# Kernel optimization log

Hardware: AMD Instinct MI355X
Metric: run time of the kernel (lower is better)

The kernel has to match this reference:

```python
import jax, jax.numpy as jnp
import numpy as np

HEAD = 16
EMD = 1024
QK = 64
V = 64
B, SQ, SKV = 4, 2048, 2048


def setup_inputs() -> dict:
    key = jax.random.key(0)
    ks = jax.random.split(key, 10)
    s = 0.02
    return {
        "x_q": jax.random.normal(ks[0], (B, SQ, EMD), dtype=jnp.float32),
        "x_k_v": jax.random.normal(ks[1], (B, SKV, EMD), dtype=jnp.float32),
        "mask_pad": jax.random.randint(ks[2], (B, SQ, SKV), 0, 2) > 0,
        # torch nn.Linear weights: [out_features, in_features]
        "Wq_w": jax.random.normal(ks[3], (QK * HEAD, EMD), dtype=jnp.float32) * s,
        "Wq_b": jnp.zeros((QK * HEAD,), dtype=jnp.float32),
        "Wk_w": jax.random.normal(ks[4], (QK * HEAD, EMD), dtype=jnp.float32) * s,
        "Wk_b": jnp.zeros((QK * HEAD,), dtype=jnp.float32),
        "Wv_w": jax.random.normal(ks[5], (V * HEAD, EMD), dtype=jnp.float32) * s,
        "Wv_b": jnp.zeros((V * HEAD,), dtype=jnp.float32),
    }


def reference(x_q, x_k_v, mask_pad, Wq_w, Wq_b, Wk_w, Wk_b, Wv_w, Wv_b):
    b, sq, _ = x_q.shape
    skv = x_k_v.shape[1]
    q = x_q @ Wq_w.T + Wq_b            # [B, SQ, H*QK]
    k = x_k_v @ Wk_w.T + Wk_b          # [B, SKV, H*QK]
    v = x_k_v @ Wv_w.T + Wv_b          # [B, SKV, H*V]
    q = q.reshape(b, sq, HEAD, QK).transpose(0, 2, 1, 3)   # [B, H, SQ, QK]
    k = k.reshape(b, skv, HEAD, QK).transpose(0, 2, 1, 3)  # [B, H, SKV, QK]
    v = v.reshape(b, skv, HEAD, V).transpose(0, 2, 1, 3)   # [B, H, SKV, V]
    scale = 1.0 / jnp.sqrt(jnp.float32(QK))
    atten = jnp.einsum('bhqd,bhkd->bhqk', q, k) * scale    # [B, H, SQ, SKV]
    atten = jnp.where(mask_pad[:, None, :, :], jnp.float32(-1e9), atten)
    atten = jax.nn.softmax(atten, axis=-1)
    z = jnp.einsum('bhqk,bhkv->bhqv', atten, v)            # [B, H, SQ, V]
    z = z.transpose(0, 2, 1, 3).reshape(b, sq, HEAD * V)   # [B, SQ, H*V]
    return z
```

## Files before the change

kernel.cpp:

```cpp
#include <hip/hip_runtime.h>
#include <stdint.h>

#define HEADS 16
#define EMDIM 1024
#define DHEAD 64
#define BATCH 4
#define SEQQ 2048
#define SEQK 2048
#define NT (SEQK / 64)
#define QSCALE 0.18033688011112042f

typedef __attribute__((ext_vector_type(8))) short bf16x8;
typedef __attribute__((ext_vector_type(4))) float f32x4;
typedef __attribute__((ext_vector_type(4))) unsigned int u32x4;

typedef __attribute__((address_space(3))) void lds_void;
typedef const __attribute__((address_space(1))) void gbl_void;
#define GL_LDS16(g, l) __builtin_amdgcn_global_load_lds((gbl_void*)(g), (lds_void*)(l), 16, 0, 0)
#define MFMA16(a, b, c) __builtin_amdgcn_mfma_f32_16x16x32_bf16(a, b, c, 0, 0, 0)

__device__ __forceinline__ unsigned short f2bf(float f) {
    unsigned int u = __builtin_bit_cast(unsigned int, f);
    u += 0x7fffu + ((u >> 16) & 1u);
    return (unsigned short)(u >> 16);
}

__device__ __forceinline__ void exp2x4(float& a, float& b, float& c, float& d) {
    asm("v_exp_f32 %0, %0\n\t"
        "v_exp_f32 %1, %1\n\t"
        "v_exp_f32 %2, %2\n\t"
        "v_exp_f32 %3, %3\n\t"
        "s_nop 0"
        : "+v"(a), "+v"(b), "+v"(c), "+v"(d));
}

__device__ __forceinline__ unsigned int cvtpk_bf16(float lo, float hi) {
    unsigned int r;
    asm("v_cvt_pk_bf16_f32 %0, %1, %2" : "=v"(r) : "v"(lo), "v"(hi));
    return r;
}

__global__ __launch_bounds__(256) void prep_all(const float* __restrict__ xq,
                                                const float* __restrict__ xkv,
                                                const float* __restrict__ wq,
                                                const float* __restrict__ wk,
                                                const float* __restrict__ wv,
                                                unsigned short* __restrict__ oxq,
                                                unsigned short* __restrict__ oxkv,
                                                unsigned short* __restrict__ owq,
                                                unsigned short* __restrict__ owk,
                                                unsigned short* __restrict__ owv,
                                                const void* __restrict__ mask,
                                                unsigned long long* __restrict__ packed) {
    const int NX = (BATCH * SEQQ * EMDIM) / 4;
    const int NW = (EMDIM * EMDIM) / 4;
    const int total = 2 * NX + 3 * NW;
    for (int i = blockIdx.x * 256 + threadIdx.x; i < total; i += gridDim.x * 256) {
        const float* src;
        unsigned short* dst;
        int j = i;
        if (j < NX) { src = xq; dst = oxq; }
        else if ((j -= NX) < NX) { src = xkv; dst = oxkv; }
        else if ((j -= NX) < NW) { src = wq; dst = owq; }
        else if ((j -= NW) < NW) { src = wk; dst = owk; }
        else { j -= NW; src = wv; dst = owv; }
        float4 v = reinterpret_cast<const float4*>(src)[j];
        ushort4 o;
        o.x = f2bf(v.x); o.y = f2bf(v.y); o.z = f2bf(v.z); o.w = f2bf(v.w);
        reinterpret_cast<ushort4*>(dst)[j] = o;
    }
    const int* mi = (const int*)mask;
    const uint8_t* mu = (const uint8_t*)mask;
    const int lane = threadIdx.x & 63;
    const bool u8src = __any(((unsigned)mi[lane]) > 1u);
    const size_t N = (size_t)BATCH * SEQQ * SEQK;
    const size_t stride = (size_t)gridDim.x * blockDim.x;
    for (size_t idx = (size_t)blockIdx.x * blockDim.x + threadIdx.x; idx < N; idx += stride) {
        const int v = u8src ? (int)mu[idx] : mi[idx];
        const unsigned long long bb = __ballot(v != 0);
        if (lane == 0) packed[idx >> 6] = bb;
    }
}

__global__ __launch_bounds__(256) void gemm_qkv(
    const unsigned short* __restrict__ xq, const unsigned short* __restrict__ xkv,
    const unsigned short* __restrict__ Wqm, const unsigned short* __restrict__ Wkm,
    const unsigned short* __restrict__ Wvm,
    const float* __restrict__ bq, const float* __restrict__ bk, const float* __restrict__ bv,
    unsigned short* __restrict__ Qo, unsigned short* __restrict__ Ko,
    unsigned short* __restrict__ Vo) {
    __shared__ __align__(16) unsigned short Alds[128 * 64];
    __shared__ __align__(16) unsigned short Blds[128 * 64];
    const int nb = blockIdx.x;
    const int which = nb >> 3;
    const unsigned short* A = (which == 0) ? xq : xkv;
    const unsigned short* W = (which == 0) ? Wqm : (which == 1) ? Wkm : Wvm;
    const float* bias = (which == 0) ? bq : (which == 1) ? bk : bv;
    const int n0 = (nb & 7) * 128;
    const int m0 = blockIdx.y * 128;

    const int tid = threadIdx.x;
    const int lane = tid & 63;
    const int wid = tid >> 6;
    const int wm = wid >> 1, wn = wid & 1;
    const int lq = lane & 15, lh = lane >> 4;

    f32x4 acc[4][4] = {};

    const int srow = tid >> 3;
    const int scol = (tid & 7) * 8;

    for (int kt = 0; kt < 16; ++kt) {
        const int kb = kt * 64;
#pragma unroll
        for (int i = 0; i < 4; ++i) {
            const int row = i * 32 + srow;
            GL_LDS16(&A[(size_t)(m0 + row) * EMDIM + kb + scol], &Alds[row * 64 + scol]);
            GL_LDS16(&W[(size_t)(n0 + row) * EMDIM + kb + scol], &Blds[row * 64 + scol]);
        }
        __syncthreads();
#pragma unroll
        for (int ks = 0; ks < 2; ++ks) {
            bf16x8 af[4], bfr[4];
#pragma unroll
            for (int mf = 0; mf < 4; ++mf)
                af[mf] = *(const bf16x8*)&Alds[(wm * 64 + mf * 16 + lq) * 64 + ks * 32 + lh * 8];
#pragma unroll
            for (int nf = 0; nf < 4; ++nf)
                bfr[nf] = *(const bf16x8*)&Blds[(wn * 64 + nf * 16 + lq) * 64 + ks * 32 + lh * 8];
#pragma unroll
            for (int mf = 0; mf < 4; ++mf)
#pragma unroll
                for (int nf = 0; nf < 4; ++nf)
                    acc[mf][nf] = MFMA16(af[mf], bfr[nf], acc[mf][nf]);
        }
        __syncthreads();
    }

#pragma unroll
    for (int nf = 0; nf < 4; ++nf) {
        const int n = n0 + wn * 64 + nf * 16 + lq;
        const float bvv = bias[n];
        const int h = n >> 6, d = n & 63;
#pragma unroll
        for (int mf = 0; mf < 4; ++mf) {
            const int mbase = m0 + wm * 64 + mf * 16 + lh * 4;
            const int b = mbase >> 11;
            const int s = mbase & 2047;
            if (which == 2) {
                ushort4 pk;
                pk.x = f2bf(acc[mf][nf][0] + bvv);
                pk.y = f2bf(acc[mf][nf][1] + bvv);
                pk.z = f2bf(acc[mf][nf][2] + bvv);
                pk.w = f2bf(acc[mf][nf][3] + bvv);
                *(ushort4*)&Vo[(((size_t)(b * HEADS + h) * DHEAD) + d) * SEQK + s] = pk;
            } else {
                const float sc = (which == 0) ? QSCALE : 1.0f;
                unsigned short* o = (which == 0) ? Qo : Ko;
#pragma unroll
                for (int r = 0; r < 4; ++r) {
                    float v = (acc[mf][nf][r] + bvv) * sc;
                    o[(((size_t)(b * HEADS + h) * SEQQ) + (s + r)) * DHEAD + d] = f2bf(v);
                }
            }
        }
    }
}

__global__ __launch_bounds__(256, 3) void attn_fused(const unsigned short* __restrict__ Q,
                                                     const unsigned short* __restrict__ K,
                                                     const unsigned short* __restrict__ VT,
                                                     const unsigned long long* __restrict__ mpk,
                                                     float* __restrict__ out) {
    const int tid = threadIdx.x;
    const int lane = tid & 63;
    const int wid = tid >> 6;
    const int lq = lane & 15, lh = lane >> 4;
    const int bh = blockIdx.x;
    const int b = bh >> 4, h = bh & 15;
    const int qbase = blockIdx.y * 128 + wid * 32;

    __shared__ __align__(16) unsigned short Kl[2][64 * 64];
    __shared__ __align__(16) unsigned short Vl[2][64 * 64];

    const unsigned short* Kbh = K + (size_t)bh * SEQK * DHEAD;
    const unsigned short* Vbh = VT + (size_t)bh * DHEAD * SEQK;

    bf16x8 bq[2][2];
    const unsigned long long* mrow[2];
#pragma unroll
    for (int sub = 0; sub < 2; ++sub) {
        const int q = qbase + sub * 16 + lq;
        const unsigned short* qrow = Q + ((size_t)bh * SEQQ + q) * DHEAD;
        bq[sub][0] = *(const bf16x8*)&qrow[lh * 8];
        bq[sub][1] = *(const bf16x8*)&qrow[32 + lh * 8];
        mrow[sub] = mpk + ((size_t)b * SEQQ + q) * NT;
    }

    f32x4 acc[4][2] = {};
    f32x4 accl[2] = {};

    const bf16x8 vone = {16256, 16256, 16256, 16256, 16256, 16256, 16256, 16256};

    const int srow8 = lane >> 3;
    const int sg = (lane & 7) ^ srow8;
    const int g7 = lq & 7;

    auto stage = [&](int s, int t) {
        const int k0 = t * 64;
#pragma unroll
        for (int i = 0; i < 2; ++i) {
            const int cc = wid * 2 + i;
            const int r = cc * 8 + srow8;
            GL_LDS16(Kbh + (size_t)(k0 + r) * DHEAD + sg * 8, &Kl[s][cc * 512]);
            GL_LDS16(Vbh + (size_t)r * SEQK + k0 + sg * 8, &Vl[s][cc * 512]);
        }
    };

    unsigned long long mwc[2], mwn[2];
#pragma unroll
    for (int sub = 0; sub < 2; ++sub) mwc[sub] = mrow[sub][0];

    stage(0, 0);
    __syncthreads();
    int cur = 0;

    for (int t = 0; t < NT; ++t) {
        if (t < NT - 1) {
            stage(cur ^ 1, t + 1);
#pragma unroll
            for (int sub = 0; sub < 2; ++sub) mwn[sub] = mrow[sub][t + 1];
        }

        uint2 w[2][4];
#pragma unroll
        for (int kb = 0; kb < 4; ++kb) {
            const unsigned short* kr = &Kl[cur][(kb * 16 + lq) * 64];
            const bf16x8 a0 = *(const bf16x8*)&kr[((0 + lh) ^ g7) * 8];
            const bf16x8 a1 = *(const bf16x8*)&kr[((4 + lh) ^ g7) * 8];
#pragma unroll
            for (int sub = 0; sub < 2; ++sub) {
                f32x4 z = {};
                z = MFMA16(a0, bq[sub][0], z);
                z = MFMA16(a1, bq[sub][1], z);
                const unsigned int ml = (unsigned int)(mwc[sub] >> (kb * 16 + lh * 4));
                float p0 = (ml & 1u) ? -1e9f : z[0];
                float p1 = (ml & 2u) ? -1e9f : z[1];
                float p2 = (ml & 4u) ? -1e9f : z[2];
                float p3 = (ml & 8u) ? -1e9f : z[3];
                exp2x4(p0, p1, p2, p3);
                w[sub][kb].x = cvtpk_bf16(p0, p1);
                w[sub][kb].y = cvtpk_bf16(p2, p3);
            }
        }

        bf16x8 pf[2][2];
#pragma unroll
        for (int sub = 0; sub < 2; ++sub) {
#pragma unroll
            for (int ks = 0; ks < 2; ++ks) {
                unsigned int s0 = w[sub][2 * ks].x, s2 = w[sub][2 * ks + 1].x;
                unsigned int s1 = w[sub][2 * ks].y, s3 = w[sub][2 * ks + 1].y;
                asm("v_permlane32_swap_b32 %0, %1" : "+v"(s0), "+v"(s2));
                asm("v_permlane32_swap_b32 %0, %1" : "+v"(s1), "+v"(s3));
                asm("v_permlane16_swap_b32 %0, %1" : "+v"(s0), "+v"(s2));
                asm("v_permlane16_swap_b32 %0, %1" : "+v"(s1), "+v"(s3));
                u32x4 fd = {s0, s1, s2, s3};
                pf[sub][ks] = __builtin_bit_cast(bf16x8, fd);
            }
        }

        __builtin_amdgcn_s_setprio(1);
#pragma unroll
        for (int sub = 0; sub < 2; ++sub) {
            accl[sub] = MFMA16(vone, pf[sub][0], accl[sub]);
            accl[sub] = MFMA16(vone, pf[sub][1], accl[sub]);
        }
#pragma unroll
        for (int vb = 0; vb < 4; ++vb) {
            const unsigned short* vr = &Vl[cur][(vb * 16 + lq) * 64];
            const bf16x8 av0 = *(const bf16x8*)&vr[((0 + lh) ^ g7) * 8];
            const bf16x8 av1 = *(const bf16x8*)&vr[((4 + lh) ^ g7) * 8];
#pragma unroll
            for (int sub = 0; sub < 2; ++sub) {
                acc[vb][sub] = MFMA16(av0, pf[sub][0], acc[vb][sub]);
                acc[vb][sub] = MFMA16(av1, pf[sub][1], acc[vb][sub]);
            }
        }
        __builtin_amdgcn_s_setprio(0);

        __syncthreads();
        cur ^= 1;
#pragma unroll
        for (int sub = 0; sub < 2; ++sub) mwc[sub] = mwn[sub];
    }

#pragma unroll
    for (int sub = 0; sub < 2; ++sub) {
        const float rl = 1.f / accl[sub][0];
        const int q = qbase + sub * 16 + lq;
        float* orow = out + ((size_t)b * SEQQ + q) * (HEADS * DHEAD) + h * DHEAD;
#pragma unroll
        for (int vb = 0; vb < 4; ++vb) {
            float4 o4;
            o4.x = acc[vb][sub][0] * rl;
            o4.y = acc[vb][sub][1] * rl;
            o4.z = acc[vb][sub][2] * rl;
            o4.w = acc[vb][sub][3] * rl;
            *(float4*)&orow[vb * 16 + lh * 4] = o4;
        }
    }
}

extern "C" void kernel_launch(void* const* d_in, const int* in_sizes, int n_in,
                              void* d_out, int out_size, void* d_ws, size_t ws_size,
                              hipStream_t stream) {
    const float* x_q  = (const float*)d_in[0];
    const float* x_kv = (const float*)d_in[1];
    const void*  mask = (const void*)d_in[2];
    const float* Wq_w = (const float*)d_in[3];
    const float* Wq_b = (const float*)d_in[4];
    const float* Wk_w = (const float*)d_in[5];
    const float* Wk_b = (const float*)d_in[6];
    const float* Wv_w = (const float*)d_in[7];
    const float* Wv_b = (const float*)d_in[8];
    float* out = (float*)d_out;

    char* ws = (char*)d_ws;
    const size_t SZ_QKV = (size_t)BATCH * HEADS * SEQQ * DHEAD * sizeof(unsigned short);
    const size_t SZ_X   = (size_t)BATCH * SEQQ * EMDIM * sizeof(unsigned short);
    const size_t SZ_W   = (size_t)EMDIM * EMDIM * sizeof(unsigned short);
    unsigned short* Qb  = (unsigned short*)(ws);
    unsigned short* Kb  = (unsigned short*)(ws + SZ_QKV);
    unsigned short* VTb = (unsigned short*)(ws + 2 * SZ_QKV);
    unsigned short* xqb = (unsigned short*)(ws + 3 * SZ_QKV);
    unsigned short* xkb = (unsigned short*)(ws + 3 * SZ_QKV + SZ_X);
    unsigned short* Wqb = (unsigned short*)(ws + 3 * SZ_QKV + 2 * SZ_X);
    unsigned short* Wkb = (unsigned short*)(ws + 3 * SZ_QKV + 2 * SZ_X + SZ_W);
    unsigned short* Wvb = (unsigned short*)(ws + 3 * SZ_QKV + 2 * SZ_X + 2 * SZ_W);
    unsigned long long* mpk = (unsigned long long*)(ws + 3 * SZ_QKV + 2 * SZ_X + 3 * SZ_W);

    prep_all<<<2048, 256, 0, stream>>>(x_q, x_kv, Wq_w, Wk_w, Wv_w, xqb, xkb, Wqb, Wkb, Wvb,
                                       mask, mpk);

    dim3 ggrid(24, BATCH * SEQQ / 128);
    gemm_qkv<<<ggrid, 256, 0, stream>>>(xqb, xkb, Wqb, Wkb, Wvb, Wq_b, Wk_b, Wv_b, Qb, Kb, VTb);

    dim3 agrid(BATCH * HEADS, SEQQ / 128);
    attn_fused<<<agrid, 256, 0, stream>>>(Qb, Kb, VTb, mpk, out);
}
```

Before: 219.3 us.

## Stage Q/K GEMM epilogue through swizzled LDS and remap blocks across XCDs

The Q and K outputs of the QKV projection GEMM are now written into a swizzled LDS tile first and then stored to global memory as 16-byte vectors per row. Previously each lane wrote scattered 2-byte values. Block IDs are also remapped so that consecutive M tiles land on different XCDs while N tiles of the same M tile share an XCD, aiming for better L2 reuse of the A rows. This adds an extra barrier and LDS round trip in the epilogue. The remap assumes a grid of 24 by the number of M tiles and a multiple of 8 XCDs.

```diff
diff --git a/kernel.cpp b/kernel.cpp
--- a/kernel.cpp
+++ b/kernel.cpp
@@ -89,15 +89,19 @@
     const float* __restrict__ bq, const float* __restrict__ bk, const float* __restrict__ bv,
     unsigned short* __restrict__ Qo, unsigned short* __restrict__ Ko,
     unsigned short* __restrict__ Vo) {
-    __shared__ __align__(16) unsigned short Alds[128 * 64];
-    __shared__ __align__(16) unsigned short Blds[128 * 64];
-    const int nb = blockIdx.x;
+    __shared__ __align__(16) unsigned short Tlds[2][128 * 64];
+
+    const int rawid = blockIdx.y * gridDim.x + blockIdx.x;
+    const int xcd = rawid & 7;
+    const int slot = rawid >> 3;
+    const int nb = slot % 24;
+    const int mt = (slot / 24) * 8 + xcd;
+    const int m0 = mt * 128;
     const int which = nb >> 3;
     const unsigned short* A = (which == 0) ? xq : xkv;
     const unsigned short* W = (which == 0) ? Wqm : (which == 1) ? Wkm : Wvm;
     const float* bias = (which == 0) ? bq : (which == 1) ? bk : bv;
     const int n0 = (nb & 7) * 128;
-    const int m0 = blockIdx.y * 128;
 
     const int tid = threadIdx.x;
     const int lane = tid & 63;
@@ -115,8 +119,8 @@
 #pragma unroll
         for (int i = 0; i < 4; ++i) {
             const int row = i * 32 + srow;
-            GL_LDS16(&A[(size_t)(m0 + row) * EMDIM + kb + scol], &Alds[row * 64 + scol]);
-            GL_LDS16(&W[(size_t)(n0 + row) * EMDIM + kb + scol], &Blds[row * 64 + scol]);
+            GL_LDS16(&A[(size_t)(m0 + row) * EMDIM + kb + scol], &Tlds[0][row * 64 + scol]);
+            GL_LDS16(&W[(size_t)(n0 + row) * EMDIM + kb + scol], &Tlds[1][row * 64 + scol]);
         }
         __syncthreads();
 #pragma unroll
@@ -124,10 +128,10 @@
             bf16x8 af[4], bfr[4];
 #pragma unroll
             for (int mf = 0; mf < 4; ++mf)
-                af[mf] = *(const bf16x8*)&Alds[(wm * 64 + mf * 16 + lq) * 64 + ks * 32 + lh * 8];
+                af[mf] = *(const bf16x8*)&Tlds[0][(wm * 64 + mf * 16 + lq) * 64 + ks * 32 + lh * 8];
 #pragma unroll
             for (int nf = 0; nf < 4; ++nf)
-                bfr[nf] = *(const bf16x8*)&Blds[(wn * 64 + nf * 16 + lq) * 64 + ks * 32 + lh * 8];
+                bfr[nf] = *(const bf16x8*)&Tlds[1][(wn * 64 + nf * 16 + lq) * 64 + ks * 32 + lh * 8];
 #pragma unroll
             for (int mf = 0; mf < 4; ++mf)
 #pragma unroll
@@ -137,32 +141,56 @@
         __syncthreads();
     }
 
-#pragma unroll
-    for (int nf = 0; nf < 4; ++nf) {
-        const int n = n0 + wn * 64 + nf * 16 + lq;
-        const float bvv = bias[n];
-        const int h = n >> 6, d = n & 63;
-#pragma unroll
-        for (int mf = 0; mf < 4; ++mf) {
-            const int mbase = m0 + wm * 64 + mf * 16 + lh * 4;
-            const int b = mbase >> 11;
-            const int s = mbase & 2047;
-            if (which == 2) {
+    if (which == 2) {
+#pragma unroll
+        for (int nf = 0; nf < 4; ++nf) {
+            const int n = n0 + wn * 64 + nf * 16 + lq;
+            const float bvv = bias[n];
+            const int h = n >> 6, d = n & 63;
+#pragma unroll
+            for (int mf = 0; mf < 4; ++mf) {
+                const int mbase = m0 + wm * 64 + mf * 16 + lh * 4;
+                const int b = mbase >> 11;
+                const int s = mbase & 2047;
                 ushort4 pk;
                 pk.x = f2bf(acc[mf][nf][0] + bvv);
                 pk.y = f2bf(acc[mf][nf][1] + bvv);
                 pk.z = f2bf(acc[mf][nf][2] + bvv);
                 pk.w = f2bf(acc[mf][nf][3] + bvv);
                 *(ushort4*)&Vo[(((size_t)(b * HEADS + h) * DHEAD) + d) * SEQK + s] = pk;
-            } else {
-                const float sc = (which == 0) ? QSCALE : 1.0f;
-                unsigned short* o = (which == 0) ? Qo : Ko;
+            }
+        }
+    } else {
+        unsigned short* ep = &Tlds[0][0];
+        const float sc = (which == 0) ? QSCALE : 1.0f;
+#pragma unroll
+        for (int nf = 0; nf < 4; ++nf) {
+            const int n_l = wn * 64 + nf * 16 + lq;
+            const float bvv = bias[n0 + n_l];
+            const int g = n_l >> 3;
+#pragma unroll
+            for (int mf = 0; mf < 4; ++mf) {
 #pragma unroll
                 for (int r = 0; r < 4; ++r) {
-                    float v = (acc[mf][nf][r] + bvv) * sc;
-                    o[(((size_t)(b * HEADS + h) * SEQQ) + (s + r)) * DHEAD + d] = f2bf(v);
+                    const int m_l = wm * 64 + mf * 16 + lh * 4 + r;
+                    ep[m_l * 128 + ((g ^ (m_l & 7)) << 3) + (n_l & 7)] =
+                        f2bf((acc[mf][nf][r] + bvv) * sc);
                 }
             }
+        }
+        __syncthreads();
+        unsigned short* o = (which == 0) ? Qo : Ko;
+        const int row = tid >> 1;
+        const int half = tid & 1;
+        const int b = (m0 + row) >> 11;
+        const int ss = (m0 + row) & 2047;
+        const int h = (n0 >> 6) + half;
+        unsigned short* orow = &o[(((size_t)(b * HEADS + h) * SEQQ) + ss) * DHEAD];
+#pragma unroll
+        for (int j = 0; j < 8; ++j) {
+            const int gidx = half * 8 + j;
+            const u32x4 v = *(const u32x4*)&ep[row * 128 + ((gidx ^ (row & 7)) << 3)];
+            *(u32x4*)&orow[j * 8] = v;
         }
     }
 }
```

Result: slower. 224.2 us (+2.2%).
